# Optimization experiments

Hardware: AMD Instinct MI355X
Metric: run time of the kernel (lower is better)

Reference implementation:

```python
import jax, jax.numpy as jnp
import numpy as np

RADIUS = 4  # matches init radius


def _bilinear_sample(v, grid):
    """Faithful F.grid_sample(v, grid, mode='bilinear', align_corners=True, padding_mode='zeros').
    v: (B,C,H,W); grid: (B,Hg,Wg,2) in [-1,1]; grid[...,0]->width(x), grid[...,1]->height(y)."""
    B, C, H, W = v.shape
    Hg, Wg = grid.shape[1], grid.shape[2]
    ix = (grid[..., 0] + 1.0) * 0.5 * (W - 1)
    iy = (grid[..., 1] + 1.0) * 0.5 * (H - 1)
    x0 = jnp.floor(ix); y0 = jnp.floor(iy)
    x1 = x0 + 1.0;      y1 = y0 + 1.0
    wx1 = ix - x0; wx0 = 1.0 - wx1
    wy1 = iy - y0; wy0 = 1.0 - wy1
    v_flat = v.reshape(B, C, H * W)
    out = jnp.zeros((B, C, Hg, Wg), v.dtype)
    for xf, yf, w in ((x0, y0, wx0 * wy0), (x1, y0, wx1 * wy0),
                      (x0, y1, wx0 * wy1), (x1, y1, wx1 * wy1)):
        valid = (xf >= 0) & (xf <= W - 1) & (yf >= 0) & (yf <= H - 1)
        xi = jnp.clip(xf, 0, W - 1).astype(jnp.int32)
        yi = jnp.clip(yf, 0, H - 1).astype(jnp.int32)
        idx = (yi * W + xi).reshape(B, 1, Hg * Wg)
        g = jnp.take_along_axis(v_flat, idx, axis=2).reshape(B, C, Hg, Wg)
        out = out + g * (w * valid)[:, None, :, :]
    return out


def setup_inputs() -> dict:
    key = jax.random.key(0)
    ks = jax.random.split(key, 5)
    B, C, H, W, K = 4, 128, 128, 128, 8
    x = jax.random.normal(ks[0], (B, C, H, W), jnp.float32)
    psf_tbl = jax.random.randint(ks[1], (B, H, W, K, 2), 0, 128)  # absolute pixel anchors
    delta = jax.random.normal(ks[2], (1, 1, 1, K, 2), jnp.float32) * 0.1
    w_qkv = jax.random.normal(ks[3], (3 * C, C), jnp.float32) * (C ** -0.5)  # 1x1 conv, no bias
    w_proj = jax.random.normal(ks[4], (C, C), jnp.float32) * (C ** -0.5)
    return {"x": x, "psf_tbl": psf_tbl, "delta": delta, "w_qkv": w_qkv, "w_proj": w_proj}


def reference(x, psf_tbl, delta, w_qkv, w_proj):
    B, C, H, W = x.shape
    K = psf_tbl.shape[3]
    qkv = jnp.einsum('oc,bchw->bohw', w_qkv, x)  # 1x1 conv to_qkv
    q, k, v = jnp.split(qkv, 3, axis=1)
    offsets = psf_tbl.astype(x.dtype) + jnp.tanh(delta) * RADIUS  # (B,H,W,K,2)
    norm = jnp.array([H - 1, W - 1], x.dtype)
    grid = (offsets / norm * 2.0 - 1.0).reshape(B, H, W * K, 2)
    k_s = _bilinear_sample(k, grid).reshape(B, C, H, W, K)
    v_s = _bilinear_sample(v, grid).reshape(B, C, H, W, K)
    attn = jnp.einsum('bchw,bchwk->bhwk', q, k_s) * (C ** -0.5)
    attn = jax.nn.softmax(attn, axis=-1)  # softmax over K sampled points
    out = jnp.einsum('bhwk,bchwk->bchw', attn, v_s)
    return x + jnp.einsum('oc,bchw->bohw', w_proj, out)
```

## Files before the change

### kernel.cpp

```cpp
#include <hip/hip_runtime.h>

#define HW 16384
#define C 128

typedef __attribute__((ext_vector_type(8))) short short8;
typedef __attribute__((ext_vector_type(4))) float f32x4;
typedef __attribute__((ext_vector_type(2))) float f32x2;

__device__ __forceinline__ unsigned short f2bf(float f) {
  union { float f; unsigned u; } v; v.f = f;
  return (unsigned short)((v.u + 0x7fffu + ((v.u >> 16) & 1u)) >> 16);
}
__device__ __forceinline__ float bflo(unsigned w) {
  union { unsigned u; float f; } v; v.u = w << 16; return v.f;
}
__device__ __forceinline__ float bfhi(unsigned w) {
  union { unsigned u; float f; } v; v.u = w & 0xffff0000u; return v.f;
}
__device__ __forceinline__ unsigned long long pk4(float a, float b, float c, float d) {
  return (unsigned long long)f2bf(a) | ((unsigned long long)f2bf(b) << 16) |
         ((unsigned long long)f2bf(c) << 32) | ((unsigned long long)f2bf(d) << 48);
}

__global__ void k_prep(const float* __restrict__ delta, float* __restrict__ pw,
                       int* __restrict__ pi) {
  int k = threadIdx.x;
  if (k < 8) {
    float s0 = tanhf(delta[k * 2 + 0]) * 4.0f;
    float s1 = tanhf(delta[k * 2 + 1]) * 4.0f;
    float f0 = floorf(s0), f1 = floorf(s1);
    pi[2 * k + 0] = (int)f0;
    pi[2 * k + 1] = (int)f1;
    float fx = s0 - f0, fy = s1 - f1;
    pw[4 * k + 0] = (1.0f - fx) * (1.0f - fy);
    pw[4 * k + 1] = fx * (1.0f - fy);
    pw[4 * k + 2] = (1.0f - fx) * fy;
    pw[4 * k + 3] = fx * fy;
  }
}

__global__ __launch_bounds__(256) void k_qkv(const float* __restrict__ x,
                                             const float* __restrict__ w_qkv,
                                             unsigned short* __restrict__ qb,
                                             unsigned* __restrict__ kvb) {
  __shared__ __align__(16) unsigned char smem[65536];
  unsigned short* Xs = (unsigned short*)smem;
  unsigned short* Ws = (unsigned short*)(smem + 32768);
  const int t = threadIdx.x;
  const int gpix0 = blockIdx.x * 128;
  const int b = gpix0 >> 14;
  const int hw0 = gpix0 & (HW - 1);

  const float* xb = x + (size_t)b * C * HW + hw0;
  #pragma unroll
  for (int i = 0; i < 16; ++i) {
    int linear = i * 256 + t;
    int p = linear & 127;
    int c4 = (linear >> 7) * 4;
    float a0 = xb[(size_t)(c4 + 0) * HW + p];
    float a1 = xb[(size_t)(c4 + 1) * HW + p];
    float a2 = xb[(size_t)(c4 + 2) * HW + p];
    float a3 = xb[(size_t)(c4 + 3) * HW + p];
    int cc = c4 ^ ((p & 7) << 3);
    *(unsigned long long*)&Xs[p * 128 + cc] = pk4(a0, a1, a2, a3);
  }

  const int wave = t >> 6, lane = t & 63;
  const int wr = wave >> 1, wc = wave & 1;
  const int rsel = lane & 15, quad = lane >> 4;

  if (blockIdx.y == 0) {
    #pragma unroll
    for (int i = 0; i < 16; ++i) {
      int linear = i * 256 + t;
      int c4 = (linear & 31) * 4;
      int o = linear >> 5;
      float4 w4 = *(const float4*)(w_qkv + (size_t)o * C + c4);
      *(unsigned long long*)&Ws[o * 128 + (c4 ^ ((o & 7) << 3))] = pk4(w4.x, w4.y, w4.z, w4.w);
    }
    __syncthreads();
    f32x4 acc[4][4];
    #pragma unroll
    for (int mi = 0; mi < 4; ++mi)
      #pragma unroll
      for (int ni = 0; ni < 4; ++ni) acc[mi][ni] = (f32x4){0.f, 0.f, 0.f, 0.f};
    #pragma unroll
    for (int ks = 0; ks < 4; ++ks) {
      const int koff = ks * 32 + quad * 8;
      short8 afr[4], bfr[4];
      #pragma unroll
      for (int mi = 0; mi < 4; ++mi) {
        int r = wr * 64 + mi * 16 + rsel;
        afr[mi] = *(const short8*)&Xs[r * 128 + (koff ^ ((r & 7) << 3))];
      }
      #pragma unroll
      for (int ni = 0; ni < 4; ++ni) {
        int r = wc * 64 + ni * 16 + rsel;
        bfr[ni] = *(const short8*)&Ws[r * 128 + (koff ^ ((r & 7) << 3))];
      }
      #pragma unroll
      for (int mi = 0; mi < 4; ++mi)
        #pragma unroll
        for (int ni = 0; ni < 4; ++ni)
          acc[mi][ni] = __builtin_amdgcn_mfma_f32_16x16x32_bf16(afr[mi], bfr[ni], acc[mi][ni], 0, 0, 0);
    }
    #pragma unroll
    for (int mi = 0; mi < 4; ++mi)
      #pragma unroll
      for (int ni = 0; ni < 4; ++ni)
        #pragma unroll
        for (int r = 0; r < 4; ++r) {
          int pix = gpix0 + wr * 64 + mi * 16 + quad * 4 + r;
          int ch = wc * 64 + ni * 16 + rsel;
          qb[(size_t)pix * C + ch] = f2bf(acc[mi][ni][r]);
        }
  } else {
    f32x4 acck[4][4], accv[4][4];
    #pragma unroll
    for (int mi = 0; mi < 4; ++mi)
      #pragma unroll
      for (int ni = 0; ni < 4; ++ni) {
        acck[mi][ni] = (f32x4){0.f, 0.f, 0.f, 0.f};
        accv[mi][ni] = (f32x4){0.f, 0.f, 0.f, 0.f};
      }
    #pragma unroll
    for (int ph = 0; ph < 2; ++ph) {
      if (ph == 1) __syncthreads();
      const float* wsrc = w_qkv + (size_t)(128 + ph * 128) * C;
      #pragma unroll
      for (int i = 0; i < 16; ++i) {
        int linear = i * 256 + t;
        int c4 = (linear & 31) * 4;
        int o = linear >> 5;
        float4 w4 = *(const float4*)(wsrc + (size_t)o * C + c4);
        *(unsigned long long*)&Ws[o * 128 + (c4 ^ ((o & 7) << 3))] = pk4(w4.x, w4.y, w4.z, w4.w);
      }
      __syncthreads();
      #pragma unroll
      for (int ks = 0; ks < 4; ++ks) {
        const int koff = ks * 32 + quad * 8;
        short8 afr[4], bfr[4];
        #pragma unroll
        for (int mi = 0; mi < 4; ++mi) {
          int r = wr * 64 + mi * 16 + rsel;
          afr[mi] = *(const short8*)&Ws[r * 128 + (koff ^ ((r & 7) << 3))];
        }
        #pragma unroll
        for (int ni = 0; ni < 4; ++ni) {
          int r = wc * 64 + ni * 16 + rsel;
          bfr[ni] = *(const short8*)&Xs[r * 128 + (koff ^ ((r & 7) << 3))];
        }
        #pragma unroll
        for (int mi = 0; mi < 4; ++mi)
          #pragma unroll
          for (int ni = 0; ni < 4; ++ni) {
            if (ph == 0)
              acck[mi][ni] = __builtin_amdgcn_mfma_f32_16x16x32_bf16(afr[mi], bfr[ni], acck[mi][ni], 0, 0, 0);
            else
              accv[mi][ni] = __builtin_amdgcn_mfma_f32_16x16x32_bf16(afr[mi], bfr[ni], accv[mi][ni], 0, 0, 0);
          }
      }
    }
    __syncthreads();
    unsigned* kvs = (unsigned*)smem;
    #pragma unroll
    for (int mi = 0; mi < 4; ++mi)
      #pragma unroll
      for (int ni = 0; ni < 4; ++ni) {
        int ochb = wr * 64 + mi * 16 + quad * 4;
        int pixl = wc * 64 + ni * 16 + rsel;
        unsigned d0 = (unsigned)__builtin_amdgcn_cvt_pk_fp8_f32(acck[mi][ni][0], acck[mi][ni][1], 0, false) & 0xffffu;
        d0 = (unsigned)__builtin_amdgcn_cvt_pk_fp8_f32(accv[mi][ni][0], accv[mi][ni][1], (int)d0, true);
        unsigned d1 = (unsigned)__builtin_amdgcn_cvt_pk_fp8_f32(acck[mi][ni][2], acck[mi][ni][3], 0, false) & 0xffffu;
        d1 = (unsigned)__builtin_amdgcn_cvt_pk_fp8_f32(accv[mi][ni][2], accv[mi][ni][3], (int)d1, true);
        kvs[pixl * 65 + (ochb >> 1) + 0] = d0;
        kvs[pixl * 65 + (ochb >> 1) + 1] = d1;
      }
    __syncthreads();
    #pragma unroll
    for (int i = 0; i < 32; ++i) {
      int linear = i * 256 + t;
      int p = linear >> 6;
      int d = linear & 63;
      kvb[((size_t)(gpix0 + p)) * 64 + d] = kvs[p * 65 + d];
    }
  }
}

__global__ __launch_bounds__(256) void k_attn(const unsigned short* __restrict__ qb,
                                              const unsigned* __restrict__ kvb,
                                              const int* __restrict__ psf,
                                              const float* __restrict__ pw,
                                              const int* __restrict__ pi,
                                              unsigned short* __restrict__ ao) {
  const int t = threadIdx.x;
  const int lane = t & 63;
  const int p = blockIdx.x;
  const int b = (p >> 1) & 3;
  const int j = ((p >> 3) << 1) | (p & 1);
  const int spix = __builtin_amdgcn_readfirstlane((b << 14) + (j << 2) + (t >> 6));

  const unsigned* kv32 = kvb + (size_t)b * HW * 64;

  const unsigned qp = ((const unsigned*)qb)[(size_t)spix * 64 + lane];
  const float qx = bflo(qp), qy = bfhi(qp);

  int anch[16];
  #pragma unroll
  for (int jj = 0; jj < 16; ++jj) anch[jj] = psf[(size_t)spix * 16 + jj];

  float dk[8];
  float2 vs[8];
  #pragma unroll
  for (int k = 0; k < 8; ++k) {
    const int x0 = anch[k * 2 + 0] + pi[2 * k + 0], x1 = x0 + 1;
    const int y0 = anch[k * 2 + 1] + pi[2 * k + 1], y1 = y0 + 1;
    float ksx = 0, ksy = 0, vsx = 0, vsy = 0;
    #pragma unroll
    for (int cn = 0; cn < 4; ++cn) {
      const int xi = (cn & 1) ? x1 : x0;
      const int yi = (cn & 2) ? y1 : y0;
      const bool valid = (xi >= 0) & (xi <= 127) & (yi >= 0) & (yi <= 127);
      const int xc = min(max(xi, 0), 127);
      const int yc = min(max(yi, 0), 127);
      const float wv = valid ? pw[k * 4 + cn] : 0.0f;
      const unsigned kv = kv32[(size_t)(yc * 128 + xc) * 64 + lane];
      f32x2 kp = __builtin_amdgcn_cvt_pk_f32_fp8((int)kv, false);
      f32x2 vp = __builtin_amdgcn_cvt_pk_f32_fp8((int)kv, true);
      ksx += wv * kp.x; ksy += wv * kp.y;
      vsx += wv * vp.x; vsy += wv * vp.y;
    }
    vs[k] = make_float2(vsx, vsy);
    dk[k] = qx * ksx + qy * ksy;
  }
  #pragma unroll
  for (int off = 32; off > 0; off >>= 1) {
    #pragma unroll
    for (int k = 0; k < 8; ++k) dk[k] += __shfl_xor(dk[k], off);
  }
  float lg[8];
  float m = dk[0] * 0.08838834764831845f;
  #pragma unroll
  for (int k = 0; k < 8; ++k) { lg[k] = dk[k] * 0.08838834764831845f; m = fmaxf(m, lg[k]); }
  float e[8], den = 0.0f;
  #pragma unroll
  for (int k = 0; k < 8; ++k) { e[k] = __expf(lg[k] - m); den += e[k]; }
  const float inv = 1.0f / den;
  float ox = 0, oy = 0;
  #pragma unroll
  for (int k = 0; k < 8; ++k) { float pk = e[k] * inv; ox += pk * vs[k].x; oy += pk * vs[k].y; }
  ((unsigned*)ao)[(size_t)spix * 64 + lane] = (unsigned)f2bf(ox) | ((unsigned)f2bf(oy) << 16);
}

__global__ __launch_bounds__(256) void k_proj(const unsigned short* __restrict__ ao,
                                              const float* __restrict__ w_proj,
                                              const float* __restrict__ x,
                                              float* __restrict__ out) {
  __shared__ __align__(16) unsigned short As[128 * 128];
  __shared__ __align__(16) unsigned short Ws[128 * 128];
  const int t = threadIdx.x;
  const int gpix0 = blockIdx.x * 128;
  const int b = gpix0 >> 14;
  const int hw0 = gpix0 & (HW - 1);

  #pragma unroll
  for (int i = 0; i < 8; ++i) {
    int linear = i * 256 + t;
    int c8 = (linear & 15) * 8;
    int p = linear >> 4;
    uint4 v = *(const uint4*)(ao + (size_t)(gpix0 + p) * C + c8);
    *(uint4*)&As[p * 128 + (c8 ^ ((p & 7) << 3))] = v;
  }
  #pragma unroll
  for (int i = 0; i < 16; ++i) {
    int linear = i * 256 + t;
    int c4 = (linear & 31) * 4;
    int o = linear >> 5;
    float4 w4 = *(const float4*)(w_proj + (size_t)o * C + c4);
    *(unsigned long long*)&Ws[o * 128 + (c4 ^ ((o & 7) << 3))] = pk4(w4.x, w4.y, w4.z, w4.w);
  }
  __syncthreads();

  const int wave = t >> 6, lane = t & 63;
  const int wr = wave >> 1, wc = wave & 1;
  const int rsel = lane & 15, quad = lane >> 4;

  f32x4 acc[4][4];
  #pragma unroll
  for (int mi = 0; mi < 4; ++mi)
    #pragma unroll
    for (int ni = 0; ni < 4; ++ni) acc[mi][ni] = (f32x4){0.f, 0.f, 0.f, 0.f};

  #pragma unroll
  for (int ks = 0; ks < 4; ++ks) {
    const int koff = ks * 32 + quad * 8;
    short8 afr[4], bfr[4];
    #pragma unroll
    for (int mi = 0; mi < 4; ++mi) {
      int r = wr * 64 + mi * 16 + rsel;
      afr[mi] = *(const short8*)&Ws[r * 128 + (koff ^ ((r & 7) << 3))];
    }
    #pragma unroll
    for (int ni = 0; ni < 4; ++ni) {
      int r = wc * 64 + ni * 16 + rsel;
      bfr[ni] = *(const short8*)&As[r * 128 + (koff ^ ((r & 7) << 3))];
    }
    #pragma unroll
    for (int mi = 0; mi < 4; ++mi)
      #pragma unroll
      for (int ni = 0; ni < 4; ++ni)
        acc[mi][ni] = __builtin_amdgcn_mfma_f32_16x16x32_bf16(afr[mi], bfr[ni], acc[mi][ni], 0, 0, 0);
  }

  #pragma unroll
  for (int mi = 0; mi < 4; ++mi)
    #pragma unroll
    for (int ni = 0; ni < 4; ++ni)
      #pragma unroll
      for (int r = 0; r < 4; ++r) {
        int och = wr * 64 + mi * 16 + quad * 4 + r;
        int pixl = wc * 64 + ni * 16 + rsel;
        size_t addr = ((size_t)b * C + och) * HW + hw0 + pixl;
        out[addr] = x[addr] + acc[mi][ni][r];
      }
}

extern "C" void kernel_launch(void* const* d_in, const int* in_sizes, int n_in,
                              void* d_out, int out_size, void* d_ws, size_t ws_size,
                              hipStream_t stream) {
  const float* x      = (const float*)d_in[0];
  const int*   psf    = (const int*)d_in[1];
  const float* delta  = (const float*)d_in[2];
  const float* w_qkv  = (const float*)d_in[3];
  const float* w_proj = (const float*)d_in[4];
  float* out = (float*)d_out;

  const size_t N = (size_t)4 * HW * C;
  unsigned short* qb = (unsigned short*)d_ws;
  unsigned* kvb = (unsigned*)(qb + N);
  unsigned short* ao = (unsigned short*)(kvb + (size_t)4 * HW * 64);
  float* pw = (float*)(ao + N);
  int*   pi = (int*)(pw + 32);

  k_prep<<<1, 64, 0, stream>>>(delta, pw, pi);
  k_qkv<<<dim3(512, 2), 256, 0, stream>>>(x, w_qkv, qb, kvb);
  k_attn<<<dim3(HW), 256, 0, stream>>>(qb, kvb, psf, pw, pi, ao);
  k_proj<<<dim3(512), 256, 0, stream>>>(ao, w_proj, x, out);
}
```

Before: 178.6 us.

## Merge Q and KV projection blocks and use hardware bf16 pack conversion

The QKV projection kernel previously launched two block rows, each reloading and converting the same x tile, one for Q and one for K/V. Now a single block computes Q, then K and V, reusing the staged x tile. This halves x reads and conversion work but serialises all three GEMMs in one block and halves the grid to 512 blocks. Software bf16 rounding is also replaced by the packed cvt_pk_bf16_f32 builtin where available, and the shared buffer grows slightly.

```diff
diff --git a/kernel.cpp b/kernel.cpp
--- a/kernel.cpp
+++ b/kernel.cpp
@@ -11,15 +11,26 @@
   union { float f; unsigned u; } v; v.f = f;
   return (unsigned short)((v.u + 0x7fffu + ((v.u >> 16) & 1u)) >> 16);
 }
+#if __has_builtin(__builtin_amdgcn_cvt_pk_bf16_f32)
+typedef __attribute__((ext_vector_type(2))) __bf16 bf16x2;
+__device__ __forceinline__ unsigned pk2(float a, float b) {
+  union { bf16x2 v; unsigned u; } cv;
+  cv.v = __builtin_amdgcn_cvt_pk_bf16_f32(a, b);
+  return cv.u;
+}
+#else
+__device__ __forceinline__ unsigned pk2(float a, float b) {
+  return (unsigned)f2bf(a) | ((unsigned)f2bf(b) << 16);
+}
+#endif
+__device__ __forceinline__ unsigned short f2bf1(float a) {
+  return (unsigned short)(pk2(a, a) & 0xffffu);
+}
 __device__ __forceinline__ float bflo(unsigned w) {
   union { unsigned u; float f; } v; v.u = w << 16; return v.f;
 }
 __device__ __forceinline__ float bfhi(unsigned w) {
   union { unsigned u; float f; } v; v.u = w & 0xffff0000u; return v.f;
-}
-__device__ __forceinline__ unsigned long long pk4(float a, float b, float c, float d) {
-  return (unsigned long long)f2bf(a) | ((unsigned long long)f2bf(b) << 16) |
-         ((unsigned long long)f2bf(c) << 32) | ((unsigned long long)f2bf(d) << 48);
 }
 
 __global__ void k_prep(const float* __restrict__ delta, float* __restrict__ pw,
@@ -43,7 +54,7 @@
                                              const float* __restrict__ w_qkv,
                                              unsigned short* __restrict__ qb,
                                              unsigned* __restrict__ kvb) {
-  __shared__ __align__(16) unsigned char smem[65536];
+  __shared__ __align__(16) unsigned char smem[66560];
   unsigned short* Xs = (unsigned short*)smem;
   unsigned short* Ws = (unsigned short*)(smem + 32768);
   const int t = threadIdx.x;
@@ -62,23 +73,23 @@
     float a2 = xb[(size_t)(c4 + 2) * HW + p];
     float a3 = xb[(size_t)(c4 + 3) * HW + p];
     int cc = c4 ^ ((p & 7) << 3);
-    *(unsigned long long*)&Xs[p * 128 + cc] = pk4(a0, a1, a2, a3);
+    *(uint2*)&Xs[p * 128 + cc] = make_uint2(pk2(a0, a1), pk2(a2, a3));
   }
 
   const int wave = t >> 6, lane = t & 63;
   const int wr = wave >> 1, wc = wave & 1;
   const int rsel = lane & 15, quad = lane >> 4;
 
-  if (blockIdx.y == 0) {
-    #pragma unroll
-    for (int i = 0; i < 16; ++i) {
-      int linear = i * 256 + t;
-      int c4 = (linear & 31) * 4;
-      int o = linear >> 5;
-      float4 w4 = *(const float4*)(w_qkv + (size_t)o * C + c4);
-      *(unsigned long long*)&Ws[o * 128 + (c4 ^ ((o & 7) << 3))] = pk4(w4.x, w4.y, w4.z, w4.w);
-    }
-    __syncthreads();
+  #pragma unroll
+  for (int i = 0; i < 16; ++i) {
+    int linear = i * 256 + t;
+    int c4 = (linear & 31) * 4;
+    int o = linear >> 5;
+    float4 w4 = *(const float4*)(w_qkv + (size_t)o * C + c4);
+    *(uint2*)&Ws[o * 128 + (c4 ^ ((o & 7) << 3))] = make_uint2(pk2(w4.x, w4.y), pk2(w4.z, w4.w));
+  }
+  __syncthreads();
+  {
     f32x4 acc[4][4];
     #pragma unroll
     for (int mi = 0; mi < 4; ++mi)
@@ -112,78 +123,78 @@
         for (int r = 0; r < 4; ++r) {
           int pix = gpix0 + wr * 64 + mi * 16 + quad * 4 + r;
           int ch = wc * 64 + ni * 16 + rsel;
-          qb[(size_t)pix * C + ch] = f2bf(acc[mi][ni][r]);
+          qb[(size_t)pix * C + ch] = f2bf1(acc[mi][ni][r]);
         }
-  } else {
-    f32x4 acck[4][4], accv[4][4];
-    #pragma unroll
-    for (int mi = 0; mi < 4; ++mi)
+  }
+
+  f32x4 acck[4][4], accv[4][4];
+  #pragma unroll
+  for (int mi = 0; mi < 4; ++mi)
+    #pragma unroll
+    for (int ni = 0; ni < 4; ++ni) {
+      acck[mi][ni] = (f32x4){0.f, 0.f, 0.f, 0.f};
+      accv[mi][ni] = (f32x4){0.f, 0.f, 0.f, 0.f};
+    }
+  #pragma unroll
+  for (int ph = 0; ph < 2; ++ph) {
+    __syncthreads();
+    const float* wsrc = w_qkv + (size_t)(128 + ph * 128) * C;
+    #pragma unroll
+    for (int i = 0; i < 16; ++i) {
+      int linear = i * 256 + t;
+      int c4 = (linear & 31) * 4;
+      int o = linear >> 5;
+      float4 w4 = *(const float4*)(wsrc + (size_t)o * C + c4);
+      *(uint2*)&Ws[o * 128 + (c4 ^ ((o & 7) << 3))] = make_uint2(pk2(w4.x, w4.y), pk2(w4.z, w4.w));
+    }
+    __syncthreads();
+    #pragma unroll
+    for (int ks = 0; ks < 4; ++ks) {
+      const int koff = ks * 32 + quad * 8;
+      short8 afr[4], bfr[4];
+      #pragma unroll
+      for (int mi = 0; mi < 4; ++mi) {
+        int r = wr * 64 + mi * 16 + rsel;
+        afr[mi] = *(const short8*)&Ws[r * 128 + (koff ^ ((r & 7) << 3))];
+      }
       #pragma unroll
       for (int ni = 0; ni < 4; ++ni) {
-        acck[mi][ni] = (f32x4){0.f, 0.f, 0.f, 0.f};
-        accv[mi][ni] = (f32x4){0.f, 0.f, 0.f, 0.f};
-      }
-    #pragma unroll
-    for (int ph = 0; ph < 2; ++ph) {
-      if (ph == 1) __syncthreads();
-      const float* wsrc = w_qkv + (size_t)(128 + ph * 128) * C;
-      #pragma unroll
-      for (int i = 0; i < 16; ++i) {
-        int linear = i * 256 + t;
-        int c4 = (linear & 31) * 4;
-        int o = linear >> 5;
-        float4 w4 = *(const float4*)(wsrc + (size_t)o * C + c4);
-        *(unsigned long long*)&Ws[o * 128 + (c4 ^ ((o & 7) << 3))] = pk4(w4.x, w4.y, w4.z, w4.w);
-      }
-      __syncthreads();
-      #pragma unroll
-      for (int ks = 0; ks < 4; ++ks) {
-        const int koff = ks * 32 + quad * 8;
-        short8 afr[4], bfr[4];
-        #pragma unroll
-        for (int mi = 0; mi < 4; ++mi) {
-          int r = wr * 64 + mi * 16 + rsel;
-          afr[mi] = *(const short8*)&Ws[r * 128 + (koff ^ ((r & 7) << 3))];
-        }
+        int r = wc * 64 + ni * 16 + rsel;
+        bfr[ni] = *(const short8*)&Xs[r * 128 + (koff ^ ((r & 7) << 3))];
+      }
+      #pragma unroll
+      for (int mi = 0; mi < 4; ++mi)
         #pragma unroll
         for (int ni = 0; ni < 4; ++ni) {
-          int r = wc * 64 + ni * 16 + rsel;
-          bfr[ni] = *(const short8*)&Xs[r * 128 + (koff ^ ((r & 7) << 3))];
+          if (ph == 0)
+            acck[mi][ni] = __builtin_amdgcn_mfma_f32_16x16x32_bf16(afr[mi], bfr[ni], acck[mi][ni], 0, 0, 0);
+          else
+            accv[mi][ni] = __builtin_amdgcn_mfma_f32_16x16x32_bf16(afr[mi], bfr[ni], accv[mi][ni], 0, 0, 0);
         }
-        #pragma unroll
-        for (int mi = 0; mi < 4; ++mi)
-          #pragma unroll
-          for (int ni = 0; ni < 4; ++ni) {
-            if (ph == 0)
-              acck[mi][ni] = __builtin_amdgcn_mfma_f32_16x16x32_bf16(afr[mi], bfr[ni], acck[mi][ni], 0, 0, 0);
-            else
-              accv[mi][ni] = __builtin_amdgcn_mfma_f32_16x16x32_bf16(afr[mi], bfr[ni], accv[mi][ni], 0, 0, 0);
-          }
-      }
-    }
-    __syncthreads();
-    unsigned* kvs = (unsigned*)smem;
-    #pragma unroll
-    for (int mi = 0; mi < 4; ++mi)
-      #pragma unroll
-      for (int ni = 0; ni < 4; ++ni) {
-        int ochb = wr * 64 + mi * 16 + quad * 4;
-        int pixl = wc * 64 + ni * 16 + rsel;
-        unsigned d0 = (unsigned)__builtin_amdgcn_cvt_pk_fp8_f32(acck[mi][ni][0], acck[mi][ni][1], 0, false) & 0xffffu;
-        d0 = (unsigned)__builtin_amdgcn_cvt_pk_fp8_f32(accv[mi][ni][0], accv[mi][ni][1], (int)d0, true);
-        unsigned d1 = (unsigned)__builtin_amdgcn_cvt_pk_fp8_f32(acck[mi][ni][2], acck[mi][ni][3], 0, false) & 0xffffu;
-        d1 = (unsigned)__builtin_amdgcn_cvt_pk_fp8_f32(accv[mi][ni][2], accv[mi][ni][3], (int)d1, true);
-        kvs[pixl * 65 + (ochb >> 1) + 0] = d0;
-        kvs[pixl * 65 + (ochb >> 1) + 1] = d1;
-      }
-    __syncthreads();
-    #pragma unroll
-    for (int i = 0; i < 32; ++i) {
-      int linear = i * 256 + t;
-      int p = linear >> 6;
-      int d = linear & 63;
-      kvb[((size_t)(gpix0 + p)) * 64 + d] = kvs[p * 65 + d];
-    }
+    }
+  }
+  __syncthreads();
+  unsigned* kvs = (unsigned*)smem;
+  #pragma unroll
+  for (int mi = 0; mi < 4; ++mi)
+    #pragma unroll
+    for (int ni = 0; ni < 4; ++ni) {
+      int ochb = wr * 64 + mi * 16 + quad * 4;
+      int pixl = wc * 64 + ni * 16 + rsel;
+      unsigned d0 = (unsigned)__builtin_amdgcn_cvt_pk_fp8_f32(acck[mi][ni][0], acck[mi][ni][1], 0, false) & 0xffffu;
+      d0 = (unsigned)__builtin_amdgcn_cvt_pk_fp8_f32(accv[mi][ni][0], accv[mi][ni][1], (int)d0, true);
+      unsigned d1 = (unsigned)__builtin_amdgcn_cvt_pk_fp8_f32(acck[mi][ni][2], acck[mi][ni][3], 0, false) & 0xffffu;
+      d1 = (unsigned)__builtin_amdgcn_cvt_pk_fp8_f32(accv[mi][ni][2], accv[mi][ni][3], (int)d1, true);
+      kvs[pixl * 65 + (ochb >> 1) + 0] = d0;
+      kvs[pixl * 65 + (ochb >> 1) + 1] = d1;
+    }
+  __syncthreads();
+  #pragma unroll
+  for (int i = 0; i < 32; ++i) {
+    int linear = i * 256 + t;
+    int p = linear >> 6;
+    int d = linear & 63;
+    kvb[((size_t)(gpix0 + p)) * 64 + d] = kvs[p * 65 + d];
   }
 }
 
@@ -249,7 +260,7 @@
   float ox = 0, oy = 0;
   #pragma unroll
   for (int k = 0; k < 8; ++k) { float pk = e[k] * inv; ox += pk * vs[k].x; oy += pk * vs[k].y; }
-  ((unsigned*)ao)[(size_t)spix * 64 + lane] = (unsigned)f2bf(ox) | ((unsigned)f2bf(oy) << 16);
+  ((unsigned*)ao)[(size_t)spix * 64 + lane] = pk2(ox, oy);
 }
 
 __global__ __launch_bounds__(256) void k_proj(const unsigned short* __restrict__ ao,
@@ -277,7 +288,7 @@
     int c4 = (linear & 31) * 4;
     int o = linear >> 5;
     float4 w4 = *(const float4*)(w_proj + (size_t)o * C + c4);
-    *(unsigned long long*)&Ws[o * 128 + (c4 ^ ((o & 7) << 3))] = pk4(w4.x, w4.y, w4.z, w4.w);
+    *(uint2*)&Ws[o * 128 + (c4 ^ ((o & 7) << 3))] = make_uint2(pk2(w4.x, w4.y), pk2(w4.z, w4.w));
   }
   __syncthreads();
 
@@ -343,7 +354,7 @@
   int*   pi = (int*)(pw + 32);
 
   k_prep<<<1, 64, 0, stream>>>(delta, pw, pi);
-  k_qkv<<<dim3(512, 2), 256, 0, stream>>>(x, w_qkv, qb, kvb);
+  k_qkv<<<dim3(512), 256, 0, stream>>>(x, w_qkv, qb, kvb);
   k_attn<<<dim3(HW), 256, 0, stream>>>(qb, kvb, psf, pw, pi, ao);
   k_proj<<<dim3(512), 256, 0, stream>>>(ao, w_proj, x, out);
 }
```

After: 176.8 us. Within noise of the previous version (-1.0%).
